# Optimization experiments

Hardware: AMD Instinct MI355X
Metric: run time of the kernel (lower is better)

## Reference

```python
import jax, jax.numpy as jnp
import numpy as np

INPUT_SZ = 512
HIDDEN_SZ = 512
BATCH = 64
SEQ = 512


def setup_inputs() -> dict:
    key = jax.random.key(0)
    k_x, k_ih, k_hh = jax.random.split(key, 3)
    x = jax.random.normal(k_x, (BATCH, SEQ, INPUT_SZ), dtype=jnp.float32)
    # xavier-uniform style init for 2-D params, zeros for bias (as in init_weights)
    lim_ih = float(np.sqrt(6.0 / (INPUT_SZ + 4 * HIDDEN_SZ)))
    lim_hh = float(np.sqrt(6.0 / (HIDDEN_SZ + 4 * HIDDEN_SZ)))
    weight_ih = jax.random.uniform(k_ih, (INPUT_SZ, 4 * HIDDEN_SZ), jnp.float32, -lim_ih, lim_ih)
    weight_hh = jax.random.uniform(k_hh, (HIDDEN_SZ, 4 * HIDDEN_SZ), jnp.float32, -lim_hh, lim_hh)
    bias = jnp.zeros((4 * HIDDEN_SZ,), jnp.float32)
    h0 = jnp.zeros((1, BATCH, HIDDEN_SZ), jnp.float32)
    c0 = jnp.zeros((1, BATCH, HIDDEN_SZ), jnp.float32)
    return {"x": x, "weight_ih": weight_ih, "weight_hh": weight_hh, "bias": bias, "h0": h0, "c0": c0}


def reference(x, weight_ih, weight_hh, bias, h0, c0):
    HS = weight_hh.shape[0]
    # Precompute input projection for all timesteps: (seq, batch, 4*HS)
    x_proj = jnp.einsum('bsi,ih->sbh', x, weight_ih)

    def step(carry, xp_t):
        h_t, c_t = carry  # (1, b, HS)
        gates = xp_t[None] + h_t @ weight_hh + bias  # (1, b, 4*HS)
        i_t = jax.nn.sigmoid(gates[..., :HS])
        f_t = jax.nn.sigmoid(gates[..., HS:2 * HS])
        g_t = jnp.tanh(gates[..., 2 * HS:3 * HS])
        o_t = jax.nn.sigmoid(gates[..., 3 * HS:])
        c_t = f_t * c_t + i_t * g_t
        h_t = o_t * jnp.tanh(c_t)
        return (h_t, c_t), h_t[0]  # emit (b, HS)

    (h_T, c_T), hs = jax.lax.scan(step, (h0, c0), x_proj)
    hidden_seq = jnp.transpose(hs, (1, 0, 2))  # (batch, seq, HS)
    return hidden_seq, h_T, c_T
```

## Files before the change

kernel.cpp:

```cpp
#include <hip/hip_runtime.h>

#define SEQ   512
#define BATCH 64
#define IS    512
#define HS    512
#define G4    2048

typedef _Float16 half8 __attribute__((ext_vector_type(8)));
typedef _Float16 half4 __attribute__((ext_vector_type(4)));
typedef float floatx4 __attribute__((ext_vector_type(4)));
typedef unsigned long long ull;

__device__ __forceinline__ float sigm(float x) {
    return 1.0f / (1.0f + __expf(-x));
}
__device__ __forceinline__ float tanh_(float x) {
    float e = __expf(-2.0f * fabsf(x));
    float r = (1.0f - e) / (1.0f + e);
    return copysignf(r, x);
}

__global__ void convert_f32_f16(const float* __restrict__ in,
                                _Float16* __restrict__ out, int n4) {
    int i = blockIdx.x * blockDim.x + threadIdx.x;
    if (i < n4) {
        float4 v = ((const float4*)in)[i];
        half4 o = { (_Float16)v.x, (_Float16)v.y, (_Float16)v.z, (_Float16)v.w };
        ((half4*)out)[i] = o;
    }
}

__global__ void transpose_w(const float* __restrict__ in, _Float16* __restrict__ out) {
    __shared__ _Float16 tile[64][72];
    int bk = blockIdx.x & 7;
    int bn = blockIdx.x >> 3;
    int c = threadIdx.x & 63;
    int r4 = threadIdx.x >> 6;
    #pragma unroll
    for (int rr = 0; rr < 16; rr++) {
        int k = rr * 4 + r4;
        tile[k][c] = (_Float16)in[(size_t)(bk * 64 + k) * 2048 + bn * 64 + c];
    }
    __syncthreads();
    #pragma unroll
    for (int rr = 0; rr < 16; rr++) {
        int n = rr * 4 + r4;
        out[(size_t)(bn * 64 + n) * 512 + bk * 64 + c] = tile[c][n];
    }
}

__global__ void __launch_bounds__(256, 2) gemm_xproj(
    const _Float16* __restrict__ A,
    const _Float16* __restrict__ Bt,
    _Float16* __restrict__ xp) {
    __shared__ _Float16 As[4096];
    __shared__ _Float16 Bs[4096];
    const int tid = threadIdx.x;
    const int w = tid >> 6, l = tid & 63, lr = l & 15, q = l >> 4;
    const int bm = blockIdx.x & 255, bn = blockIdx.x >> 8;
    const int row0 = bm * 128, col0 = bn * 128;
    const int wr = (w >> 1) * 64, wc = (w & 1) * 64;

    floatx4 zz = {0.f, 0.f, 0.f, 0.f};
    floatx4 acc[4][4];
    #pragma unroll
    for (int mt = 0; mt < 4; mt++)
        #pragma unroll
        for (int ct = 0; ct < 4; ct++) acc[mt][ct] = zz;

    for (int kt = 0; kt < 16; kt++) {
        __syncthreads();
        #pragma unroll
        for (int rnd = 0; rnd < 2; rnd++) {
            int o = tid * 16 + rnd * 4096;
            int r = o >> 6;
            int ke = (o & 63) >> 1;
            *(half8*)((char*)As + o) = *(const half8*)(A  + (size_t)(row0 + r) * 512 + kt * 32 + ke);
            *(half8*)((char*)Bs + o) = *(const half8*)(Bt + (size_t)(col0 + r) * 512 + kt * 32 + ke);
        }
        __syncthreads();
        half8 af[4], bf[4];
        #pragma unroll
        for (int mt = 0; mt < 4; mt++)
            af[mt] = *(const half8*)(As + (wr + mt * 16 + lr) * 32 + q * 8);
        #pragma unroll
        for (int ct = 0; ct < 4; ct++)
            bf[ct] = *(const half8*)(Bs + (wc + ct * 16 + lr) * 32 + q * 8);
        #pragma unroll
        for (int mt = 0; mt < 4; mt++)
            #pragma unroll
            for (int ct = 0; ct < 4; ct++)
                acc[mt][ct] = __builtin_amdgcn_mfma_f32_16x16x32_f16(af[mt], bf[ct], acc[mt][ct], 0, 0, 0);
    }
    #pragma unroll
    for (int mt = 0; mt < 4; mt++) {
        #pragma unroll
        for (int r = 0; r < 4; r++) {
            int row = row0 + wr + mt * 16 + q * 4 + r;
            int t = row & 511, b = row >> 9;
            #pragma unroll
            for (int ct = 0; ct < 4; ct++) {
                int col = col0 + wc + ct * 16 + lr;
                int hid = col & 511, gate = col >> 9;
                int wgd = hid >> 4, u = hid & 15;
                xp[(size_t)(((t * 32 + wgd) * 64 + b)) * 64 + u * 4 + gate] =
                    (_Float16)acc[mt][ct][r];
            }
        }
    }
}

__global__ void __launch_bounds__(256, 1) lstm_scan(
    const _Float16* __restrict__ xp,
    const _Float16* __restrict__ wt,
    _Float16* __restrict__ hb,
    const float* __restrict__ bias,
    const float* __restrict__ h0,
    const float* __restrict__ c0,
    float* __restrict__ out) {
    __shared__ _Float16 wlds[16384];
    __shared__ _Float16 scr[4 * 320];
    const int wg = blockIdx.x;
    const int tid = threadIdx.x;
    const int w = tid >> 6;
    const int l = tid & 63;
    const int lr = l & 15;
    const int q = l >> 4;
    const int myhid = wg * 16 + lr;
    _Float16* scrw = scr + w * 320;
    const ull POISON = ~0ull;

    for (int idx = tid; idx < 2048; idx += 256) {
        int n = idx >> 6, g = idx & 63;
        int gate = n >> 4, u = n & 15;
        half8 v = *(const half8*)(wt + (size_t)(gate * 512 + wg * 16 + u) * 512 + g * 8);
        *(half8*)(wlds + n * 512 + ((g ^ (n & 7)) * 8)) = v;
    }
    half8 wreg[16][2];
    #pragma unroll
    for (int kt = 0; kt < 16; kt++)
        #pragma unroll
        for (int gg = 0; gg < 2; gg++)
            wreg[kt][gg] = *(const half8*)(wt + (size_t)((2 + gg) * 512 + wg * 16 + lr) * 512 + kt * 32 + q * 8);

    {
        int b = tid >> 2, u4 = (tid & 3) * 4;
        union { _Float16 h[4]; ull u; } pk;
        #pragma unroll
        for (int k2 = 0; k2 < 4; k2++)
            pk.h[k2] = (_Float16)h0[b * 512 + wg * 16 + u4 + k2];
        __hip_atomic_store((ull*)hb + wg * 256 + tid, pk.u,
                           __ATOMIC_RELAXED, __HIP_MEMORY_SCOPE_AGENT);
    }

    float bs[4], c[4];
    #pragma unroll
    for (int g4 = 0; g4 < 4; g4++) bs[g4] = bias[g4 * 512 + myhid];
    #pragma unroll
    for (int r = 0; r < 4; r++) c[r] = c0[(w * 16 + q * 4 + r) * 512 + myhid];

    __syncthreads();

    int pr = 0, pw = 1, pp = 2;
    for (int t = 0; t < 512; t++) {
        half4 xv[4];
        #pragma unroll
        for (int r = 0; r < 4; r++) {
            int b = w * 16 + q * 4 + r;
            xv[r] = *(const half4*)(xp + (((size_t)t * 32 + wg) * 64 + b) * 64 + lr * 4);
        }

        const ull* hsrc = (const ull*)hb + (size_t)pr * 8192;
        const int b0 = w * 16 + lr;
        union HU { ull u[2]; half8 v; } a[16];
        int stale;
        do {
            stale = 0;
            #pragma unroll
            for (int kt = 0; kt < 16; kt++) {
                int idx = (2 * kt + (q >> 1)) * 256 + b0 * 4 + (q & 1) * 2;
                ull u0 = __hip_atomic_load(hsrc + idx,     __ATOMIC_RELAXED, __HIP_MEMORY_SCOPE_AGENT);
                ull u1 = __hip_atomic_load(hsrc + idx + 1, __ATOMIC_RELAXED, __HIP_MEMORY_SCOPE_AGENT);
                a[kt].u[0] = u0;
                a[kt].u[1] = u1;
                stale |= (int)(u0 == POISON) | (int)(u1 == POISON);
            }
        } while (stale);

        floatx4 zz = {0.f, 0.f, 0.f, 0.f};
        floatx4 acc[4] = {zz, zz, zz, zz};
        floatx4 acc2[4] = {zz, zz, zz, zz};
        #pragma unroll
        for (int kt = 0; kt < 16; kt++) {
            half8 bL[2];
            #pragma unroll
            for (int g4 = 0; g4 < 2; g4++) {
                int n = g4 * 16 + lr;
                bL[g4] = *(const half8*)(wlds + n * 512 + (((kt * 4 + q) ^ (n & 7)) * 8));
            }
            if ((kt & 1) == 0) {
                acc[0] = __builtin_amdgcn_mfma_f32_16x16x32_f16(a[kt].v, bL[0], acc[0], 0, 0, 0);
                acc[1] = __builtin_amdgcn_mfma_f32_16x16x32_f16(a[kt].v, bL[1], acc[1], 0, 0, 0);
                acc[2] = __builtin_amdgcn_mfma_f32_16x16x32_f16(a[kt].v, wreg[kt][0], acc[2], 0, 0, 0);
                acc[3] = __builtin_amdgcn_mfma_f32_16x16x32_f16(a[kt].v, wreg[kt][1], acc[3], 0, 0, 0);
            } else {
                acc2[0] = __builtin_amdgcn_mfma_f32_16x16x32_f16(a[kt].v, bL[0], acc2[0], 0, 0, 0);
                acc2[1] = __builtin_amdgcn_mfma_f32_16x16x32_f16(a[kt].v, bL[1], acc2[1], 0, 0, 0);
                acc2[2] = __builtin_amdgcn_mfma_f32_16x16x32_f16(a[kt].v, wreg[kt][0], acc2[2], 0, 0, 0);
                acc2[3] = __builtin_amdgcn_mfma_f32_16x16x32_f16(a[kt].v, wreg[kt][1], acc2[3], 0, 0, 0);
            }
        }

        float hv[4];
        #pragma unroll
        for (int r = 0; r < 4; r++) {
            float gi = acc[0][r] + acc2[0][r] + (float)xv[r][0] + bs[0];
            float gf = acc[1][r] + acc2[1][r] + (float)xv[r][1] + bs[1];
            float gg = acc[2][r] + acc2[2][r] + (float)xv[r][2] + bs[2];
            float go = acc[3][r] + acc2[3][r] + (float)xv[r][3] + bs[3];
            float i_ = sigm(gi), f_ = sigm(gf), gv = tanh_(gg), o_ = sigm(go);
            c[r] = f_ * c[r] + i_ * gv;
            float h = o_ * tanh_(c[r]);
            hv[r] = h;
            scrw[(q * 4 + r) * 20 + lr] = (_Float16)h;
        }
        asm volatile("s_waitcnt lgkmcnt(0)" ::: "memory");
        union { half4 h; ull u; } pk;
        pk.h = *(const half4*)(scrw + (l >> 2) * 20 + (l & 3) * 4);

        asm volatile("s_waitcnt vmcnt(0)" ::: "memory");

        __hip_atomic_store((ull*)hb + (size_t)pw * 8192 + wg * 256 + w * 64 + l, pk.u,
                           __ATOMIC_RELAXED, __HIP_MEMORY_SCOPE_AGENT);
        __hip_atomic_store((ull*)hb + (size_t)pp * 8192 + wg * 256 + w * 64 + l, POISON,
                           __ATOMIC_RELAXED, __HIP_MEMORY_SCOPE_AGENT);

        #pragma unroll
        for (int r = 0; r < 4; r++) {
            int b = w * 16 + q * 4 + r;
            out[(size_t)b * 262144 + (size_t)t * 512 + myhid] = hv[r];
            if (t == 511) {
                out[16777216 + b * 512 + myhid] = hv[r];
                out[16777216 + 32768 + b * 512 + myhid] = c[r];
            }
        }

        int tmp = pr; pr = pw; pw = pp; pp = tmp;
    }
}

extern "C" void kernel_launch(void* const* d_in, const int* in_sizes, int n_in,
                              void* d_out, int out_size, void* d_ws, size_t ws_size,
                              hipStream_t stream) {
    const float* x    = (const float*)d_in[0];
    const float* wih  = (const float*)d_in[1];
    const float* whh  = (const float*)d_in[2];
    const float* bias = (const float*)d_in[3];
    const float* h0   = (const float*)d_in[4];
    const float* c0   = (const float*)d_in[5];
    float* out = (float*)d_out;

    char* ws = (char*)d_ws;
    _Float16* x16  = (_Float16*)(ws);
    _Float16* wtih = (_Float16*)(ws + 33554432);
    _Float16* wthh = (_Float16*)(ws + 35651584);
    _Float16* xp   = (_Float16*)(ws + 37748736);
    _Float16* hb   = (_Float16*)(ws + 33554432);

    convert_f32_f16<<<16384, 256, 0, stream>>>(x, x16, BATCH * SEQ * IS / 4);
    transpose_w<<<256, 256, 0, stream>>>(wih, wtih);
    transpose_w<<<256, 256, 0, stream>>>(whh, wthh);
    gemm_xproj<<<4096, 256, 0, stream>>>(x16, wtih, xp);
    hipMemsetAsync(hb, 0xFF, 196608, stream);
    lstm_scan<<<32, 256, 0, stream>>>(xp, wthh, hb, bias, h0, c0, out);
}
```

Baseline: 2.331 ms.

## Split LSTM scan across 128 single-wave blocks with per-batch-group counter barriers

The recurrent scan moves from 32 blocks of 4 waves to 128 one-wave blocks, each owning 16 hidden units for one 16-row batch group. Batch groups become independent chains that only synchronize among their own 32 blocks. The poison-value polling of the hidden-state buffer is replaced by per-group atomic counters on separate cache lines, with a double-buffered h layout. The x-projection layout is reordered to match. This is meant to shrink each step's synchronization domain and spread the work over more CUs, at the cost of reloading the weights in 4x as many blocks and adding counter atomics.

```diff
diff --git a/kernel.cpp b/kernel.cpp
--- a/kernel.cpp
+++ b/kernel.cpp
@@ -102,38 +102,38 @@
             for (int ct = 0; ct < 4; ct++) {
                 int col = col0 + wc + ct * 16 + lr;
                 int hid = col & 511, gate = col >> 9;
-                int wgd = hid >> 4, u = hid & 15;
-                xp[(size_t)(((t * 32 + wgd) * 64 + b)) * 64 + u * 4 + gate] =
+                int wgd = (b >> 4) * 32 + (hid >> 4);
+                int bl = b & 15, u = hid & 15;
+                xp[(size_t)(((t * 128 + wgd) * 16 + bl)) * 64 + u * 4 + gate] =
                     (_Float16)acc[mt][ct][r];
             }
         }
     }
 }
 
-__global__ void __launch_bounds__(256, 1) lstm_scan(
+__global__ void __launch_bounds__(64, 1) lstm_scan(
     const _Float16* __restrict__ xp,
     const _Float16* __restrict__ wt,
     _Float16* __restrict__ hb,
     const float* __restrict__ bias,
     const float* __restrict__ h0,
     const float* __restrict__ c0,
-    float* __restrict__ out) {
+    float* __restrict__ out,
+    int* __restrict__ cnt) {
     __shared__ _Float16 wlds[16384];
-    __shared__ _Float16 scr[4 * 320];
+    __shared__ _Float16 scr[320];
     const int wg = blockIdx.x;
-    const int tid = threadIdx.x;
-    const int w = tid >> 6;
-    const int l = tid & 63;
+    const int bg = wg >> 5;
+    const int hg = wg & 31;
+    const int l  = threadIdx.x;
     const int lr = l & 15;
-    const int q = l >> 4;
-    const int myhid = wg * 16 + lr;
-    _Float16* scrw = scr + w * 320;
-    const ull POISON = ~0ull;
-
-    for (int idx = tid; idx < 2048; idx += 256) {
+    const int q  = l >> 4;
+    const int myhid = hg * 16 + lr;
+
+    for (int idx = l; idx < 2048; idx += 64) {
         int n = idx >> 6, g = idx & 63;
         int gate = n >> 4, u = n & 15;
-        half8 v = *(const half8*)(wt + (size_t)(gate * 512 + wg * 16 + u) * 512 + g * 8);
+        half8 v = *(const half8*)(wt + (size_t)(gate * 512 + hg * 16 + u) * 512 + g * 8);
         *(half8*)(wlds + n * 512 + ((g ^ (n & 7)) * 8)) = v;
     }
     half8 wreg[16][2];
@@ -141,15 +141,15 @@
     for (int kt = 0; kt < 16; kt++)
         #pragma unroll
         for (int gg = 0; gg < 2; gg++)
-            wreg[kt][gg] = *(const half8*)(wt + (size_t)((2 + gg) * 512 + wg * 16 + lr) * 512 + kt * 32 + q * 8);
+            wreg[kt][gg] = *(const half8*)(wt + (size_t)((2 + gg) * 512 + hg * 16 + lr) * 512 + kt * 32 + q * 8);
 
     {
-        int b = tid >> 2, u4 = (tid & 3) * 4;
+        int b = l >> 2, u4 = (l & 3) * 4;
         union { _Float16 h[4]; ull u; } pk;
         #pragma unroll
         for (int k2 = 0; k2 < 4; k2++)
-            pk.h[k2] = (_Float16)h0[b * 512 + wg * 16 + u4 + k2];
-        __hip_atomic_store((ull*)hb + wg * 256 + tid, pk.u,
+            pk.h[k2] = (_Float16)h0[(bg * 16 + b) * 512 + hg * 16 + u4 + k2];
+        __hip_atomic_store((ull*)hb + bg * 2048 + b * 128 + hg * 4 + (l & 3), pk.u,
                            __ATOMIC_RELAXED, __HIP_MEMORY_SCOPE_AGENT);
     }
 
@@ -157,35 +157,35 @@
     #pragma unroll
     for (int g4 = 0; g4 < 4; g4++) bs[g4] = bias[g4 * 512 + myhid];
     #pragma unroll
-    for (int r = 0; r < 4; r++) c[r] = c0[(w * 16 + q * 4 + r) * 512 + myhid];
-
-    __syncthreads();
-
-    int pr = 0, pw = 1, pp = 2;
+    for (int r = 0; r < 4; r++) c[r] = c0[(bg * 16 + q * 4 + r) * 512 + myhid];
+
+    asm volatile("s_waitcnt vmcnt(0)" ::: "memory");
+    if (l == 0)
+        __hip_atomic_fetch_add(&cnt[(bg * 8 + (hg & 7)) * 32], 1,
+                               __ATOMIC_RELAXED, __HIP_MEMORY_SCOPE_AGENT);
+
+    int* const cline = &cnt[(bg * 8 + (l & 7)) * 32];
+
     for (int t = 0; t < 512; t++) {
         half4 xv[4];
         #pragma unroll
-        for (int r = 0; r < 4; r++) {
-            int b = w * 16 + q * 4 + r;
-            xv[r] = *(const half4*)(xp + (((size_t)t * 32 + wg) * 64 + b) * 64 + lr * 4);
-        }
-
-        const ull* hsrc = (const ull*)hb + (size_t)pr * 8192;
-        const int b0 = w * 16 + lr;
+        for (int r = 0; r < 4; r++)
+            xv[r] = *(const half4*)(xp + (((size_t)t * 128 + wg) * 16 + q * 4 + r) * 64 + lr * 4);
+
+        const int tgt = 4 * (t + 1);
+        while (!__all(__hip_atomic_load(cline, __ATOMIC_RELAXED,
+                                        __HIP_MEMORY_SCOPE_AGENT) >= tgt)) { }
+        asm volatile("" ::: "memory");
+        __builtin_amdgcn_sched_barrier(0);
+
+        const ull* hsrc = (const ull*)hb + (size_t)((t & 1) * 4 + bg) * 2048;
         union HU { ull u[2]; half8 v; } a[16];
-        int stale;
-        do {
-            stale = 0;
-            #pragma unroll
-            for (int kt = 0; kt < 16; kt++) {
-                int idx = (2 * kt + (q >> 1)) * 256 + b0 * 4 + (q & 1) * 2;
-                ull u0 = __hip_atomic_load(hsrc + idx,     __ATOMIC_RELAXED, __HIP_MEMORY_SCOPE_AGENT);
-                ull u1 = __hip_atomic_load(hsrc + idx + 1, __ATOMIC_RELAXED, __HIP_MEMORY_SCOPE_AGENT);
-                a[kt].u[0] = u0;
-                a[kt].u[1] = u1;
-                stale |= (int)(u0 == POISON) | (int)(u1 == POISON);
-            }
-        } while (stale);
+        #pragma unroll
+        for (int kt = 0; kt < 16; kt++) {
+            int idx = lr * 128 + kt * 8 + q * 2;
+            a[kt].u[0] = __hip_atomic_load(hsrc + idx,     __ATOMIC_RELAXED, __HIP_MEMORY_SCOPE_AGENT);
+            a[kt].u[1] = __hip_atomic_load(hsrc + idx + 1, __ATOMIC_RELAXED, __HIP_MEMORY_SCOPE_AGENT);
+        }
 
         floatx4 zz = {0.f, 0.f, 0.f, 0.f};
         floatx4 acc[4] = {zz, zz, zz, zz};
@@ -222,30 +222,29 @@
             c[r] = f_ * c[r] + i_ * gv;
             float h = o_ * tanh_(c[r]);
             hv[r] = h;
-            scrw[(q * 4 + r) * 20 + lr] = (_Float16)h;
+            scr[(q * 4 + r) * 20 + lr] = (_Float16)h;
         }
         asm volatile("s_waitcnt lgkmcnt(0)" ::: "memory");
         union { half4 h; ull u; } pk;
-        pk.h = *(const half4*)(scrw + (l >> 2) * 20 + (l & 3) * 4);
-
+        pk.h = *(const half4*)(scr + (l >> 2) * 20 + (l & 3) * 4);
+
+        __hip_atomic_store((ull*)hb + (size_t)(((t + 1) & 1) * 4 + bg) * 2048
+                               + (l >> 2) * 128 + hg * 4 + (l & 3), pk.u,
+                           __ATOMIC_RELAXED, __HIP_MEMORY_SCOPE_AGENT);
         asm volatile("s_waitcnt vmcnt(0)" ::: "memory");
-
-        __hip_atomic_store((ull*)hb + (size_t)pw * 8192 + wg * 256 + w * 64 + l, pk.u,
-                           __ATOMIC_RELAXED, __HIP_MEMORY_SCOPE_AGENT);
-        __hip_atomic_store((ull*)hb + (size_t)pp * 8192 + wg * 256 + w * 64 + l, POISON,
-                           __ATOMIC_RELAXED, __HIP_MEMORY_SCOPE_AGENT);
+        if (l == 0)
+            __hip_atomic_fetch_add(&cnt[(bg * 8 + (hg & 7)) * 32], 1,
+                                   __ATOMIC_RELAXED, __HIP_MEMORY_SCOPE_AGENT);
 
         #pragma unroll
         for (int r = 0; r < 4; r++) {
-            int b = w * 16 + q * 4 + r;
+            int b = bg * 16 + q * 4 + r;
             out[(size_t)b * 262144 + (size_t)t * 512 + myhid] = hv[r];
             if (t == 511) {
                 out[16777216 + b * 512 + myhid] = hv[r];
                 out[16777216 + 32768 + b * 512 + myhid] = c[r];
             }
         }
-
-        int tmp = pr; pr = pw; pw = pp; pp = tmp;
     }
 }
 
@@ -265,12 +264,13 @@
     _Float16* wtih = (_Float16*)(ws + 33554432);
     _Float16* wthh = (_Float16*)(ws + 35651584);
     _Float16* xp   = (_Float16*)(ws + 37748736);
-    _Float16* hb   = (_Float16*)(ws + 33554432);
+    _Float16* hb   = (_Float16*)(ws + 171966464);
+    int*      cnt  = (int*)(ws + 172097536);
 
     convert_f32_f16<<<16384, 256, 0, stream>>>(x, x16, BATCH * SEQ * IS / 4);
     transpose_w<<<256, 256, 0, stream>>>(wih, wtih);
     transpose_w<<<256, 256, 0, stream>>>(whh, wthh);
     gemm_xproj<<<4096, 256, 0, stream>>>(x16, wtih, xp);
-    hipMemsetAsync(hb, 0xFF, 196608, stream);
-    lstm_scan<<<32, 256, 0, stream>>>(xp, wthh, hb, bias, h0, c0, out);
-}
+    hipMemsetAsync(cnt, 0, 4096, stream);
+    lstm_scan<<<128, 64, 0, stream>>>(xp, wthh, hb, bias, h0, c0, out, cnt);
+}
```

Result: faster. 2.096 ms (-10.1%).
